# Performance work log

Hardware: AMD Instinct MI355X
Metric: run time of the kernel (lower is better)

The kernel has to match this reference:

```python
import jax, jax.numpy as jnp
import numpy as np

# GeoFormer.generate_proposal constants (cfg.threshold_ins, cfg.min_pts_num,
# instance classes start at semantic id 4 on ScanNet)
THRESHOLD = 0.5
MIN_PTS_NUM = 50
MIN_INST_CLASS = 4


def setup_inputs() -> dict:
    key = jax.random.key(0)
    k1, k2, k3, k4 = jax.random.split(key, 4)
    B, Q, N, C = 4, 128, 50000, 20
    mask_logits = jax.random.normal(k1, (B, Q, N), dtype=jnp.float32)
    cls_logits = jax.random.normal(k2, (B, Q, C), dtype=jnp.float32)
    seg_pred = jax.random.randint(k3, (B, N), 0, C, dtype=jnp.int64)
    fg_idxs = jax.random.randint(k4, (B * N,), 0, 300000, dtype=jnp.int64)
    return {"mask_logits": mask_logits, "cls_logits": cls_logits,
            "seg_pred": seg_pred, "fg_idxs": fg_idxs}


def reference(mask_logits, cls_logits, seg_pred, fg_idxs):
    # mask_logits: [B, Q, N]  per-query point-mask logits (dense form of the
    #   per-batch list in the original; batch_offsets become the B dim)
    # cls_logits:  [B, Q, C]  per-query class logits
    # seg_pred:    [B, N]     per-point semantic prediction
    # fg_idxs:     [B*N]      foreground -> original point id map
    B, Q, N = mask_logits.shape
    m = jax.nn.sigmoid(mask_logits)                         # [B, Q, N]
    cls_pred = jnp.argmax(cls_logits, axis=2)               # [B, Q]

    # (mask_logit_b[n] > threshold) & (seg_pred == cls_logits_pred[b, n])
    sel = (m > THRESHOLD) & (seg_pred[:, None, :] == cls_pred[:, :, None])  # [B,Q,N]
    cnt = sel.sum(axis=-1)                                  # [B, Q] proposal sizes

    # score = mean of sigmoid over selected points
    msel = jnp.where(sel, m, jnp.zeros((), m.dtype))
    scores = msel.sum(axis=-1) / jnp.maximum(cnt, 1).astype(m.dtype)  # [B, Q]

    # skip if too few points or a background/wall class (< 4)
    valid = (cnt >= MIN_PTS_NUM) & (cls_pred >= MIN_INST_CLASS)       # [B, Q]

    proposal_masks = sel & valid[:, :, None]                # dense proposal_idx
    scores = jnp.where(valid, scores, jnp.zeros((), scores.dtype))
    global_ids = fg_idxs.reshape(B, N)                      # fg_idxs remap per point
    return proposal_masks, scores, valid, cls_pred, global_ids
```

## Files before the change

kernel.cpp:

```cpp
#include <hip/hip_runtime.h>
#include <math.h>

#define BB 4
#define QQ 128
#define NN 50000
#define CC 20
#define ROWS (BB * QQ)
#define NV4 (NN / 4)
#define TPB 256
#define UNROLL 4
#define BPR 13
#define WPR 1568
#define THRESH_CNT 50
#define MIN_CLS 4

typedef float f32x4 __attribute__((ext_vector_type(4)));
typedef int   i32x4 __attribute__((ext_vector_type(4)));

struct Ws {
    float sum[ROWS];
    int   cnt[ROWS];
    int   cls[ROWS];
    int   valid[ROWS];
};

__global__ void k0_argmax_zero(const float* __restrict__ cls_logits, Ws* ws) {
    int r = blockIdx.x * blockDim.x + threadIdx.x;
    if (r >= ROWS) return;
    const float* p = cls_logits + r * CC;
    float best = p[0];
    int bi = 0;
    #pragma unroll
    for (int c = 1; c < CC; ++c) {
        float v = p[c];
        if (v > best) { best = v; bi = c; }
    }
    ws->cls[r] = bi;
    ws->sum[r] = 0.0f;
    ws->cnt[r] = 0;
}


__global__ __launch_bounds__(256) void k1_pack(
        const float* __restrict__ mask_logits,
        const int*   __restrict__ seg_pred,
        unsigned int* __restrict__ bits,
        Ws* __restrict__ ws) {
    const int row = blockIdx.y;
    const int b   = row >> 7;
    const int cls = ws->cls[row];

    const f32x4* __restrict__ ml = (const f32x4*)mask_logits + (size_t)row * NV4;
    const i32x4* __restrict__ sp = (const i32x4*)seg_pred + b * NV4;

    const int base = blockIdx.x * (TPB * UNROLL) + threadIdx.x * UNROLL;

    f32x4 v[UNROLL];
    i32x4 s[UNROLL];
    bool  act[UNROLL];
    #pragma unroll
    for (int j = 0; j < UNROLL; ++j) {
        act[j] = (base + j) < NV4;
        if (act[j]) {
            v[j] = ml[base + j];
            s[j] = sp[base + j];
        }
    }

    unsigned int b16 = 0;
    float lsum = 0.0f;
    int   lcnt = 0;
    #pragma unroll
    for (int j = 0; j < UNROLL; ++j) {
        if (act[j]) {
            f32x4 vv = v[j];
            i32x4 ss = s[j];
            unsigned s0 = (vv.x > 0.0f) & (ss.x == cls);
            unsigned s1 = (vv.y > 0.0f) & (ss.y == cls);
            unsigned s2 = (vv.z > 0.0f) & (ss.z == cls);
            unsigned s3 = (vv.w > 0.0f) & (ss.w == cls);
            b16 |= (s0 | (s1 << 1) | (s2 << 2) | (s3 << 3)) << (4 * j);
            float g0 = 1.0f / (1.0f + __expf(-vv.x));
            float g1 = 1.0f / (1.0f + __expf(-vv.y));
            float g2 = 1.0f / (1.0f + __expf(-vv.z));
            float g3 = 1.0f / (1.0f + __expf(-vv.w));
            lsum += (s0 ? g0 : 0.0f) + (s1 ? g1 : 0.0f)
                  + (s2 ? g2 : 0.0f) + (s3 ? g3 : 0.0f);
            lcnt += (int)(s0 + s1 + s2 + s3);
        }
    }

    unsigned int partner = __shfl_xor((int)b16, 1);
    if ((threadIdx.x & 1) == 0) {
        unsigned int word = b16 | (partner << 16);
        const int h = blockIdx.x * TPB + threadIdx.x;
        const int w = h >> 1;
        if (w < WPR) bits[(size_t)row * WPR + w] = word;
    }

    #pragma unroll
    for (int off = 32; off > 0; off >>= 1) {
        lsum += __shfl_down(lsum, off);
        lcnt += __shfl_down(lcnt, off);
    }
    __shared__ float ssum[4];
    __shared__ int   scnt[4];
    const int wave = threadIdx.x >> 6;
    const int lane = threadIdx.x & 63;
    if (lane == 0) { ssum[wave] = lsum; scnt[wave] = lcnt; }
    __syncthreads();
    if (threadIdx.x == 0) {
        float ts = ssum[0] + ssum[1] + ssum[2] + ssum[3];
        int   tc = scnt[0] + scnt[1] + scnt[2] + scnt[3];
        atomicAdd(&ws->sum[row], ts);
        atomicAdd(&ws->cnt[row], tc);
    }
}

__global__ __launch_bounds__(256) void k_expand(
        const unsigned int* __restrict__ bits,
        const Ws* __restrict__ ws,
        float* __restrict__ out_mask) {
    const int row = blockIdx.y;
    const float on = ws->valid[row] ? 1.0f : 0.0f;
    const unsigned int* __restrict__ wb = bits + (size_t)row * WPR;
    f32x4* __restrict__ om = (f32x4*)out_mask + (size_t)row * NV4;
    const int idx0 = blockIdx.x * (TPB * UNROLL) + threadIdx.x;
    #pragma unroll
    for (int j = 0; j < UNROLL; ++j) {
        int idx = idx0 + j * TPB;
        if (idx < NV4) {
            unsigned int word = wb[idx >> 3];
            unsigned int nib = word >> ((idx & 7) * 4);
            f32x4 o;
            o.x = (nib & 1u) ? on : 0.0f;
            o.y = (nib & 2u) ? on : 0.0f;
            o.z = (nib & 4u) ? on : 0.0f;
            o.w = (nib & 8u) ? on : 0.0f;
            __builtin_nontemporal_store(o, &om[idx]);
        }
    }
}

__global__ void k2_finalize_gids(const int* __restrict__ fg,
                                 float* __restrict__ out,
                                 Ws* __restrict__ ws) {
    const int idx = blockIdx.x * blockDim.x + threadIdx.x;
    if (idx < ROWS) {
        int   cnt = ws->cnt[idx];
        int   cls = ws->cls[idx];
        float sum = ws->sum[idx];
        int valid = (cnt >= THRESH_CNT) && (cls >= MIN_CLS);
        ws->valid[idx] = valid;
        float* tail = out + (size_t)ROWS * NN;
        tail[idx]            = valid ? (sum / (float)max(cnt, 1)) : 0.0f;
        tail[ROWS + idx]     = valid ? 1.0f : 0.0f;
        tail[2 * ROWS + idx] = (float)cls;
    }
    const int nv4 = (BB * NN) / 4;
    if (idx < nv4) {
        float* gids = out + (size_t)ROWS * NN + 3 * ROWS;
        i32x4 v = ((const i32x4*)fg)[idx];
        f32x4 o;
        o.x = (float)v.x; o.y = (float)v.y; o.z = (float)v.z; o.w = (float)v.w;
        __builtin_nontemporal_store(o, &((f32x4*)gids)[idx]);
    }
}


__global__ __launch_bounds__(256) void k1_select_fused(
        const float* __restrict__ mask_logits,
        const int*   __restrict__ seg_pred,
        float* __restrict__ out_mask,
        Ws* __restrict__ ws) {
    const int row = blockIdx.y;
    const int b   = row >> 7;
    const int cls = ws->cls[row];
    const f32x4* __restrict__ ml = (const f32x4*)(mask_logits + (size_t)row * NN);
    const i32x4* __restrict__ sp = (const i32x4*)(seg_pred + b * NN);
    f32x4* __restrict__ om = (f32x4*)(out_mask + (size_t)row * NN);
    const int idx0 = blockIdx.x * (TPB * UNROLL) + threadIdx.x;
    float lsum = 0.0f;
    int   lcnt = 0;
    #pragma unroll
    for (int j = 0; j < UNROLL; ++j) {
        int idx = idx0 + j * TPB;
        if (idx >= NV4) continue;
        f32x4 vv = ml[idx];
        i32x4 ss = sp[idx];
        bool s0 = (vv.x > 0.0f) & (ss.x == cls);
        bool s1 = (vv.y > 0.0f) & (ss.y == cls);
        bool s2 = (vv.z > 0.0f) & (ss.z == cls);
        bool s3 = (vv.w > 0.0f) & (ss.w == cls);
        f32x4 o;
        o.x = s0 ? 1.0f : 0.0f;
        o.y = s1 ? 1.0f : 0.0f;
        o.z = s2 ? 1.0f : 0.0f;
        o.w = s3 ? 1.0f : 0.0f;
        lsum += (s0 ? 1.0f / (1.0f + __expf(-vv.x)) : 0.0f)
              + (s1 ? 1.0f / (1.0f + __expf(-vv.y)) : 0.0f)
              + (s2 ? 1.0f / (1.0f + __expf(-vv.z)) : 0.0f)
              + (s3 ? 1.0f / (1.0f + __expf(-vv.w)) : 0.0f);
        lcnt += (int)s0 + (int)s1 + (int)s2 + (int)s3;
        __builtin_nontemporal_store(o, &om[idx]);
    }
    #pragma unroll
    for (int off = 32; off > 0; off >>= 1) {
        lsum += __shfl_down(lsum, off);
        lcnt += __shfl_down(lcnt, off);
    }
    __shared__ float ssum[4];
    __shared__ int   scnt[4];
    const int wave = threadIdx.x >> 6;
    const int lane = threadIdx.x & 63;
    if (lane == 0) { ssum[wave] = lsum; scnt[wave] = lcnt; }
    __syncthreads();
    if (threadIdx.x == 0) {
        atomicAdd(&ws->sum[row], ssum[0] + ssum[1] + ssum[2] + ssum[3]);
        atomicAdd(&ws->cnt[row], scnt[0] + scnt[1] + scnt[2] + scnt[3]);
    }
}

__global__ __launch_bounds__(256) void k3_fixup(
        float* __restrict__ out_mask, const Ws* __restrict__ ws) {
    const int row = blockIdx.y;
    if (ws->valid[row]) return;
    f32x4* __restrict__ om = (f32x4*)(out_mask + (size_t)row * NN);
    const f32x4 z = {0.0f, 0.0f, 0.0f, 0.0f};
    const int idx0 = blockIdx.x * (TPB * UNROLL) + threadIdx.x;
    #pragma unroll
    for (int j = 0; j < UNROLL; ++j) {
        int idx = idx0 + j * TPB;
        if (idx < NV4) __builtin_nontemporal_store(z, &om[idx]);
    }
}

extern "C" void kernel_launch(void* const* d_in, const int* in_sizes, int n_in,
                              void* d_out, int out_size, void* d_ws, size_t ws_size,
                              hipStream_t stream) {
    const float* mask_logits = (const float*)d_in[0];
    const float* cls_logits  = (const float*)d_in[1];
    const int*   seg_pred    = (const int*)d_in[2];
    const int*   fg_idxs     = (const int*)d_in[3];

    float* out = (float*)d_out;
    Ws* ws = (Ws*)d_ws;
    unsigned int* bits = (unsigned int*)((char*)d_ws + sizeof(Ws));

    float* out_mask = out;

    const size_t ws_needed = sizeof(Ws) + (size_t)ROWS * WPR * sizeof(unsigned int);
    const bool use_split = (ws_size >= ws_needed);

    k0_argmax_zero<<<(ROWS + 255) / 256, 256, 0, stream>>>(cls_logits, ws);

    dim3 g1(BPR, ROWS);
    const int gids_blocks = ((BB * NN) / 4 + 255) / 256;

    if (use_split) {
        k1_pack<<<g1, TPB, 0, stream>>>(mask_logits, seg_pred, bits, ws);
        k2_finalize_gids<<<gids_blocks, 256, 0, stream>>>(fg_idxs, out, ws);
        k_expand<<<g1, TPB, 0, stream>>>(bits, ws, out_mask);
    } else {
        k1_select_fused<<<g1, TPB, 0, stream>>>(mask_logits, seg_pred, out_mask, ws);
        k2_finalize_gids<<<gids_blocks, 256, 0, stream>>>(fg_idxs, out, ws);
        k3_fixup<<<g1, TPB, 0, stream>>>(out_mask, ws);
    }
}
```

Before: 206.4 us.

## Precompute per-class seg bitmasks and pack selection bits with coalesced loads

Adds a pre-pass that turns seg_pred into one bitmask per (batch, class) using wave ballots. The pack kernel then reads a single 32-bit word per 8 float4s instead of a full int4 of seg_pred for every float4 of logits. That cuts seg_pred read traffic in the main pass by roughly 32x. The pack kernel also switches to strided (coalesced) indexing and assembles the selection words with xor-shuffles. In exchange it adds one kernel launch and more workspace, and the use_split path now only runs if that larger workspace is available.

```diff
diff --git a/kernel.cpp b/kernel.cpp
--- a/kernel.cpp
+++ b/kernel.cpp
@@ -10,7 +10,7 @@
 #define TPB 256
 #define UNROLL 4
 #define BPR 13
-#define WPR 1568
+#define W32 1568
 #define THRESH_CNT 50
 #define MIN_CLS 4
 
@@ -40,62 +40,72 @@
     ws->cnt[r] = 0;
 }
 
+__global__ void k_pre_classbit(const int* __restrict__ seg,
+                               unsigned int* __restrict__ classbit) {
+    const int b = blockIdx.y;
+    const int p = blockIdx.x * TPB + threadIdx.x;
+    const int lane = threadIdx.x & 63;
+    const int cl = (p < NN) ? seg[b * NN + p] : -1;
+    const int w0 = (blockIdx.x * TPB + (threadIdx.x & ~63)) >> 5;
+    #pragma unroll
+    for (int c = 0; c < CC; ++c) {
+        unsigned long long m = __ballot(cl == c);
+        if (lane == 0)
+            classbit[((size_t)b * CC + c) * W32 + w0]     = (unsigned int)m;
+        if (lane == 32)
+            classbit[((size_t)b * CC + c) * W32 + w0 + 1] = (unsigned int)(m >> 32);
+    }
+}
 
 __global__ __launch_bounds__(256) void k1_pack(
         const float* __restrict__ mask_logits,
-        const int*   __restrict__ seg_pred,
-        unsigned int* __restrict__ bits,
+        const unsigned int* __restrict__ classbit,
+        unsigned int* __restrict__ selbits,
         Ws* __restrict__ ws) {
     const int row = blockIdx.y;
     const int b   = row >> 7;
     const int cls = ws->cls[row];
 
+    const unsigned int* __restrict__ cb = classbit + ((size_t)b * CC + cls) * W32;
     const f32x4* __restrict__ ml = (const f32x4*)mask_logits + (size_t)row * NV4;
-    const i32x4* __restrict__ sp = (const i32x4*)seg_pred + b * NV4;
-
-    const int base = blockIdx.x * (TPB * UNROLL) + threadIdx.x * UNROLL;
-
-    f32x4 v[UNROLL];
-    i32x4 s[UNROLL];
-    bool  act[UNROLL];
-    #pragma unroll
-    for (int j = 0; j < UNROLL; ++j) {
-        act[j] = (base + j) < NV4;
-        if (act[j]) {
-            v[j] = ml[base + j];
-            s[j] = sp[base + j];
-        }
-    }
-
-    unsigned int b16 = 0;
+
+    const int tid = threadIdx.x;
+    const f32x4 vz = {0.0f, 0.0f, 0.0f, 0.0f};
+
+    f32x4        v[UNROLL];
+    unsigned int cw[UNROLL];
+    int          idx[UNROLL];
+    #pragma unroll
+    for (int j = 0; j < UNROLL; ++j) {
+        idx[j] = blockIdx.x * (TPB * UNROLL) + j * TPB + tid;
+        bool a = idx[j] < NV4;
+        v[j]  = a ? ml[idx[j]] : vz;
+        cw[j] = a ? cb[idx[j] >> 3] : 0u;
+    }
+
     float lsum = 0.0f;
     int   lcnt = 0;
     #pragma unroll
     for (int j = 0; j < UNROLL; ++j) {
-        if (act[j]) {
-            f32x4 vv = v[j];
-            i32x4 ss = s[j];
-            unsigned s0 = (vv.x > 0.0f) & (ss.x == cls);
-            unsigned s1 = (vv.y > 0.0f) & (ss.y == cls);
-            unsigned s2 = (vv.z > 0.0f) & (ss.z == cls);
-            unsigned s3 = (vv.w > 0.0f) & (ss.w == cls);
-            b16 |= (s0 | (s1 << 1) | (s2 << 2) | (s3 << 3)) << (4 * j);
-            float g0 = 1.0f / (1.0f + __expf(-vv.x));
-            float g1 = 1.0f / (1.0f + __expf(-vv.y));
-            float g2 = 1.0f / (1.0f + __expf(-vv.z));
-            float g3 = 1.0f / (1.0f + __expf(-vv.w));
-            lsum += (s0 ? g0 : 0.0f) + (s1 ? g1 : 0.0f)
-                  + (s2 ? g2 : 0.0f) + (s3 ? g3 : 0.0f);
-            lcnt += (int)(s0 + s1 + s2 + s3);
+        f32x4 vv = v[j];
+        unsigned int nib = (cw[j] >> ((tid & 7) * 4)) & 0xFu;
+        unsigned int se = ((vv.x > 0.0f) ? 1u : 0u) | ((vv.y > 0.0f) ? 2u : 0u)
+                        | ((vv.z > 0.0f) ? 4u : 0u) | ((vv.w > 0.0f) ? 8u : 0u);
+        unsigned int sel = se & nib;
+        lsum += ((sel & 1u) ? 1.0f / (1.0f + __expf(-vv.x)) : 0.0f)
+              + ((sel & 2u) ? 1.0f / (1.0f + __expf(-vv.y)) : 0.0f)
+              + ((sel & 4u) ? 1.0f / (1.0f + __expf(-vv.z)) : 0.0f)
+              + ((sel & 8u) ? 1.0f / (1.0f + __expf(-vv.w)) : 0.0f);
+        lcnt += __popc(sel);
+
+        unsigned int w = sel << (4 * (tid & 7));
+        w |= (unsigned int)__shfl_xor((int)w, 1);
+        w |= (unsigned int)__shfl_xor((int)w, 2);
+        w |= (unsigned int)__shfl_xor((int)w, 4);
+        if ((tid & 7) == 0) {
+            int wi = idx[j] >> 3;
+            if (wi < W32) selbits[(size_t)row * W32 + wi] = w;
         }
-    }
-
-    unsigned int partner = __shfl_xor((int)b16, 1);
-    if ((threadIdx.x & 1) == 0) {
-        unsigned int word = b16 | (partner << 16);
-        const int h = blockIdx.x * TPB + threadIdx.x;
-        const int w = h >> 1;
-        if (w < WPR) bits[(size_t)row * WPR + w] = word;
     }
 
     #pragma unroll
@@ -105,40 +115,13 @@
     }
     __shared__ float ssum[4];
     __shared__ int   scnt[4];
-    const int wave = threadIdx.x >> 6;
-    const int lane = threadIdx.x & 63;
+    const int wave = tid >> 6;
+    const int lane = tid & 63;
     if (lane == 0) { ssum[wave] = lsum; scnt[wave] = lcnt; }
     __syncthreads();
-    if (threadIdx.x == 0) {
-        float ts = ssum[0] + ssum[1] + ssum[2] + ssum[3];
-        int   tc = scnt[0] + scnt[1] + scnt[2] + scnt[3];
-        atomicAdd(&ws->sum[row], ts);
-        atomicAdd(&ws->cnt[row], tc);
-    }
-}
-
-__global__ __launch_bounds__(256) void k_expand(
-        const unsigned int* __restrict__ bits,
-        const Ws* __restrict__ ws,
-        float* __restrict__ out_mask) {
-    const int row = blockIdx.y;
-    const float on = ws->valid[row] ? 1.0f : 0.0f;
-    const unsigned int* __restrict__ wb = bits + (size_t)row * WPR;
-    f32x4* __restrict__ om = (f32x4*)out_mask + (size_t)row * NV4;
-    const int idx0 = blockIdx.x * (TPB * UNROLL) + threadIdx.x;
-    #pragma unroll
-    for (int j = 0; j < UNROLL; ++j) {
-        int idx = idx0 + j * TPB;
-        if (idx < NV4) {
-            unsigned int word = wb[idx >> 3];
-            unsigned int nib = word >> ((idx & 7) * 4);
-            f32x4 o;
-            o.x = (nib & 1u) ? on : 0.0f;
-            o.y = (nib & 2u) ? on : 0.0f;
-            o.z = (nib & 4u) ? on : 0.0f;
-            o.w = (nib & 8u) ? on : 0.0f;
-            __builtin_nontemporal_store(o, &om[idx]);
-        }
+    if (tid == 0) {
+        atomicAdd(&ws->sum[row], ssum[0] + ssum[1] + ssum[2] + ssum[3]);
+        atomicAdd(&ws->cnt[row], scnt[0] + scnt[1] + scnt[2] + scnt[3]);
     }
 }
 
@@ -164,6 +147,31 @@
         f32x4 o;
         o.x = (float)v.x; o.y = (float)v.y; o.z = (float)v.z; o.w = (float)v.w;
         __builtin_nontemporal_store(o, &((f32x4*)gids)[idx]);
+    }
+}
+
+__global__ __launch_bounds__(256) void k_expand(
+        const unsigned int* __restrict__ selbits,
+        const Ws* __restrict__ ws,
+        float* __restrict__ out_mask) {
+    const int row = blockIdx.y;
+    const float on = ws->valid[row] ? 1.0f : 0.0f;
+    const unsigned int* __restrict__ wb = selbits + (size_t)row * W32;
+    f32x4* __restrict__ om = (f32x4*)out_mask + (size_t)row * NV4;
+    const int idx0 = blockIdx.x * (TPB * UNROLL) + threadIdx.x;
+    #pragma unroll
+    for (int j = 0; j < UNROLL; ++j) {
+        int idx = idx0 + j * TPB;
+        if (idx < NV4) {
+            unsigned int word = wb[idx >> 3];
+            unsigned int nib = word >> ((idx & 7) * 4);
+            f32x4 o;
+            o.x = (nib & 1u) ? on : 0.0f;
+            o.y = (nib & 2u) ? on : 0.0f;
+            o.z = (nib & 4u) ? on : 0.0f;
+            o.w = (nib & 8u) ? on : 0.0f;
+            __builtin_nontemporal_store(o, &om[idx]);
+        }
     }
 }
 
@@ -245,11 +253,14 @@
 
     float* out = (float*)d_out;
     Ws* ws = (Ws*)d_ws;
-    unsigned int* bits = (unsigned int*)((char*)d_ws + sizeof(Ws));
+    unsigned int* selbits  = (unsigned int*)((char*)d_ws + sizeof(Ws));
+    unsigned int* classbit = selbits + (size_t)ROWS * W32;
 
     float* out_mask = out;
 
-    const size_t ws_needed = sizeof(Ws) + (size_t)ROWS * WPR * sizeof(unsigned int);
+    const size_t ws_needed = sizeof(Ws)
+        + (size_t)ROWS * W32 * sizeof(unsigned int)
+        + (size_t)BB * CC * W32 * sizeof(unsigned int);
     const bool use_split = (ws_size >= ws_needed);
 
     k0_argmax_zero<<<(ROWS + 255) / 256, 256, 0, stream>>>(cls_logits, ws);
@@ -258,9 +269,11 @@
     const int gids_blocks = ((BB * NN) / 4 + 255) / 256;
 
     if (use_split) {
-        k1_pack<<<g1, TPB, 0, stream>>>(mask_logits, seg_pred, bits, ws);
+        dim3 gp((NN + TPB - 1) / TPB, BB);
+        k_pre_classbit<<<gp, TPB, 0, stream>>>(seg_pred, classbit);
+        k1_pack<<<g1, TPB, 0, stream>>>(mask_logits, classbit, selbits, ws);
         k2_finalize_gids<<<gids_blocks, 256, 0, stream>>>(fg_idxs, out, ws);
-        k_expand<<<g1, TPB, 0, stream>>>(bits, ws, out_mask);
+        k_expand<<<g1, TPB, 0, stream>>>(selbits, ws, out_mask);
     } else {
         k1_select_fused<<<g1, TPB, 0, stream>>>(mask_logits, seg_pred, out_mask, ws);
         k2_finalize_gids<<<gids_blocks, 256, 0, stream>>>(fg_idxs, out, ws);
```

Result: faster. 198.9 us (-3.6%).
